# Kernel optimization log

Hardware: AMD Instinct MI355X
Metric: run time of the kernel (lower is better)

The kernel has to match this reference:

```python
import jax, jax.numpy as jnp
import numpy as np

B, S, D = 4, 2048, 1024
H, A = 16, 64  # num_heads, attention_depth
LN_EPS = 1e-3  # keras LayerNormalization default epsilon


def setup_inputs() -> dict:
    key = jax.random.key(0)
    ks = jax.random.split(key, 12)
    s_in = 1.0 / np.sqrt(D)
    return {
        "query_inputs": jax.random.normal(ks[0], (B, S, D), jnp.float32),
        "key_value_inputs": jax.random.normal(ks[1], (B, S, D), jnp.float32),
        "Wq": jax.random.normal(ks[2], (H, D, A), jnp.float32) * s_in,
        "bq": jnp.zeros((H, A), jnp.float32),
        "Wk": jax.random.normal(ks[3], (H, D, A), jnp.float32) * s_in,
        "bk": jnp.zeros((H, A), jnp.float32),
        "Wo": jax.random.normal(ks[4], (H, D, D), jnp.float32) * s_in,
        "bo": jnp.zeros((H, D), jnp.float32),
        "gamma": jnp.ones((D,), jnp.float32),
        "beta": jnp.zeros((D,), jnp.float32),
    }


def reference(query_inputs, key_value_inputs, Wq, bq, Wk, bk, Wo, bo, gamma, beta):
    sqrt_depth = jnp.sqrt(jnp.asarray(A, jnp.float32))
    # per-head Q/K projections, batched over heads: [B,H,S,A]
    q = (jnp.einsum("bsd,hda->bhsa", query_inputs, Wq) + bq[None, :, None, :]) / sqrt_depth
    k = jnp.einsum("btd,hda->bhta", key_value_inputs, Wk) + bk[None, :, None, :]
    # keras Attention: scores = q @ k^T (q already pre-scaled), causal mask
    scores = jnp.einsum("bhsa,bhta->bhst", q, k)
    causal = jnp.tril(jnp.ones((S, S), bool))
    scores = jnp.where(causal[None, None], scores, jnp.finfo(scores.dtype).min)
    weights = jax.nn.softmax(scores, axis=-1)
    # values are the raw key_value_inputs (model_dims channels)
    attn = jnp.einsum("bhst,btd->bhsd", weights, key_value_inputs)
    # per-head output dense with relu, then sum over heads (tf.add_n)
    head_out = jax.nn.relu(jnp.einsum("bhsd,hde->bhse", attn, Wo) + bo[None, :, None, :])
    attn_sum = head_out.sum(axis=1)  # [B,S,D]
    # dropout is identity in inference mode (training=False)
    x = query_inputs + attn_sum
    mean = x.mean(axis=-1, keepdims=True)
    var = x.var(axis=-1, keepdims=True)
    return gamma * (x - mean) * jax.lax.rsqrt(var + LN_EPS) + beta
```

## Files before the change

kernel.cpp:

```cpp
#include <hip/hip_runtime.h>
#include <stdint.h>

#define B_ 4
#define S_ 2048
#define D_ 1024
#define H_ 16
#define A_ 64
#define LN_EPS 1e-3f
#define L2E 1.4426950408889634f

typedef __bf16 bf16x8 __attribute__((ext_vector_type(8)));
typedef __bf16 bf16x4 __attribute__((ext_vector_type(4)));
typedef float f32x4 __attribute__((ext_vector_type(4)));

__device__ __forceinline__ f32x4 mfma16(bf16x8 a, bf16x8 b, f32x4 c) {
    return __builtin_amdgcn_mfma_f32_16x16x32_bf16(a, b, c, 0, 0, 0);
}
__device__ __forceinline__ void glds16(const void* g, void* l) {
    __builtin_amdgcn_global_load_lds(
        (const __attribute__((address_space(1))) void*)g,
        (__attribute__((address_space(3))) void*)l, 16, 0, 0);
}

#define SWZ(slot, r) ((slot) ^ (((r) & 1) << 2) ^ (((r) >> 1) & 3))
__device__ __forceinline__ void stage_half(const __bf16* __restrict__ src, size_t ld,
                                           __bf16* lhalf, int w, int lane) {
    #pragma unroll
    for (int i = 0; i < 2; ++i) {
        int ch = w * 2 + i;
        int r = ch * 8 + (lane >> 3);
        int sl = SWZ(lane & 7, r);
        glds16(src + (size_t)r * ld + sl * 8, lhalf + ch * 512);
    }
}
__device__ __forceinline__ bf16x8 fragS(const __bf16* h, int r, int ks, int fg) {
    return *(const bf16x8*)(h + r * 64 + SWZ(ks * 4 + fg, r) * 8);
}

__device__ __forceinline__ void glds_tile128(const __bf16* __restrict__ src, size_t ld,
                                             __bf16* lds, int w, int lane) {
    int r = lane >> 2;
    int c = (lane & 3) * 8;
    #pragma unroll
    for (int i = 0; i < 2; ++i) {
        int r0 = (w + i * 4) * 16;
        glds16(src + (size_t)(r0 + r) * ld + c, lds + r0 * 32);
    }
}
template <int NI, int NJ>
__device__ __forceinline__ void mfma_tileL(const __bf16* As, const __bf16* Bs,
                                           int wm, int wn, int fr, int fg,
                                           f32x4 (&acc)[NI][NJ]) {
    bf16x8 af[NI], bv[NJ];
    #pragma unroll
    for (int i = 0; i < NI; ++i)
        af[i] = *(const bf16x8*)(As + (wm + i * 16 + fr) * 32 + fg * 8);
    #pragma unroll
    for (int j = 0; j < NJ; ++j)
        bv[j] = *(const bf16x8*)(Bs + (wn + j * 16 + fr) * 32 + fg * 8);
    #pragma unroll
    for (int i = 0; i < NI; ++i)
        #pragma unroll
        for (int j = 0; j < NJ; ++j)
            acc[i][j] = mfma16(af[i], bv[j], acc[i][j]);
}

__global__ void k_tr_cvt(const float* __restrict__ in, __bf16* __restrict__ out,
                         int R, int C) {
    __shared__ float tile[32][33];
    size_t gbase = (size_t)blockIdx.z * R * C;
    int r0 = blockIdx.y * 32, c0 = blockIdx.x * 32;
    #pragma unroll
    for (int i = threadIdx.y; i < 32; i += 8)
        tile[i][threadIdx.x] = in[gbase + (size_t)(r0 + i) * C + c0 + threadIdx.x];
    __syncthreads();
    #pragma unroll
    for (int i = threadIdx.y; i < 32; i += 8)
        out[gbase + (size_t)(c0 + i) * R + r0 + threadIdx.x] = (__bf16)tile[threadIdx.x][i];
}
__global__ void k_tr_cvt2(const float* __restrict__ in0, const float* __restrict__ in1,
                          __bf16* __restrict__ out0, __bf16* __restrict__ out1,
                          int R, int C) {
    __shared__ float tile[32][33];
    int z = blockIdx.z;
    const float* in = (z < H_) ? in0 : in1;
    __bf16* out = (z < H_) ? out0 : out1;
    size_t gbase = (size_t)(z & (H_ - 1)) * R * C;
    int r0 = blockIdx.y * 32, c0 = blockIdx.x * 32;
    #pragma unroll
    for (int i = threadIdx.y; i < 32; i += 8)
        tile[i][threadIdx.x] = in[gbase + (size_t)(r0 + i) * C + c0 + threadIdx.x];
    __syncthreads();
    #pragma unroll
    for (int i = threadIdx.y; i < 32; i += 8)
        out[gbase + (size_t)(c0 + i) * R + r0 + threadIdx.x] = (__bf16)tile[threadIdx.x][i];
}

__global__ void k_cvt2(const float* __restrict__ in0, const float* __restrict__ in1,
                       __bf16* __restrict__ out0, __bf16* __restrict__ out1, int n8) {
    int i = blockIdx.x * blockDim.x + threadIdx.x;
    if (i >= n8) return;
    const float* in = blockIdx.y ? in1 : in0;
    __bf16* out = blockIdx.y ? out1 : out0;
    const float4* p = (const float4*)(in + (size_t)i * 8);
    float4 f0 = p[0], f1 = p[1];
    __bf16 v[8] = {(__bf16)f0.x, (__bf16)f0.y, (__bf16)f0.z, (__bf16)f0.w,
                   (__bf16)f1.x, (__bf16)f1.y, (__bf16)f1.z, (__bf16)f1.w};
    *(uint4*)(out + (size_t)i * 8) = *(const uint4*)v;
}

__global__ __launch_bounds__(256) void k_proj(
    const __bf16* __restrict__ qb, const __bf16* __restrict__ kvb,
    const __bf16* __restrict__ wqt, const __bf16* __restrict__ wkt,
    const float* __restrict__ bq, const float* __restrict__ bk,
    __bf16* __restrict__ qp, __bf16* __restrict__ kp) {
    __shared__ __bf16 As[2][128 * 32];
    __shared__ __bf16 Bs[2][128 * 32];
    int which = blockIdx.z;
    const __bf16* Ab = which ? kvb : qb;
    const __bf16* Bt = which ? wkt : wqt;
    const float* bias = which ? bk : bq;
    float scale = which ? 1.0f : 0.125f;
    __bf16* outp = which ? kp : qp;
    int m0 = blockIdx.y * 128, n0 = blockIdx.x * 128;
    int t = threadIdx.x, lane = t & 63, w = t >> 6;
    int wm = (w >> 1) * 64, wn = (w & 1) * 64;
    int fr = lane & 15, fg = lane >> 4;
    const __bf16* Abase = Ab + (size_t)m0 * D_;
    const __bf16* Bbase = Bt + (size_t)n0 * D_;
    f32x4 acc[4][4] = {};
    glds_tile128(Abase, D_, As[0], w, lane);
    glds_tile128(Bbase, D_, Bs[0], w, lane);
    __syncthreads();
    int cur = 0;
    const int nt = D_ / 32;
    for (int tt = 0; tt < nt; ++tt) {
        if (tt + 1 < nt) {
            glds_tile128(Abase + (tt + 1) * 32, D_, As[cur ^ 1], w, lane);
            glds_tile128(Bbase + (tt + 1) * 32, D_, Bs[cur ^ 1], w, lane);
        }
        mfma_tileL<4, 4>(As[cur], Bs[cur], wm, wn, fr, fg, acc);
        __syncthreads();
        cur ^= 1;
    }
    #pragma unroll
    for (int j = 0; j < 4; ++j) {
        int n = n0 + wn + j * 16 + fr;
        float bv = bias[n];
        #pragma unroll
        for (int i = 0; i < 4; ++i)
            #pragma unroll
            for (int jj = 0; jj < 4; ++jj) {
                int m = m0 + wm + i * 16 + fg * 4 + jj;
                outp[(size_t)m * (H_ * A_) + n] = (__bf16)((acc[i][j][jj] + bv) * scale);
            }
    }
}

__global__ __launch_bounds__(512) void k_fattn(
    const __bf16* __restrict__ qpb, const __bf16* __restrict__ kpb,
    const __bf16* __restrict__ kvtb, __bf16* __restrict__ att, int hb0) {
    __shared__ __bf16 Ks[2][64 * 64];
    __shared__ __bf16 Vs[2][2][128 * 64];
    __shared__ __bf16 Ps[128 * 64];
    __shared__ float lpar[128][2];
    int hl = blockIdx.z;
    int h = hb0 + hl;
    int yp = blockIdx.y;
    int n0 = blockIdx.x * 256;
    int t = threadIdx.x, lane = t & 63, w = t >> 6;
    int fr = lane & 15, fg = lane >> 4;
    int wr = w >> 2, wc = w & 3;
    int sr = w >> 1, sc = w & 1;
    const __bf16* Vb = kvtb + (size_t)n0 * S_;
    __bf16* ob = att + (size_t)hl * S_ * D_;

    #pragma unroll 1
    for (int seg = 0; seg < 2; ++seg) {
        int mt = seg ? (15 - yp) : yp;
        int m0 = mt * 128;
        int NT = (mt + 1) * 2;
        stage_half(qpb + (size_t)m0 * (H_ * A_) + h * A_, H_ * A_, Ps, w, lane);
        {
            int r = w * 8 + (lane >> 3);
            glds16(kpb + (size_t)r * (H_ * A_) + h * A_ + SWZ(lane & 7, r) * 8,
                   &Ks[0][w * 512]);
        }
        asm volatile("s_waitcnt vmcnt(0)" ::: "memory");
        __builtin_amdgcn_s_barrier();
        bf16x8 qf[2][2];
        #pragma unroll
        for (int mi = 0; mi < 2; ++mi)
            #pragma unroll
            for (int ks = 0; ks < 2; ++ks)
                qf[mi][ks] = fragS(Ps, sr * 32 + mi * 16 + fr, ks, fg);
        asm volatile("s_waitcnt lgkmcnt(0)" ::: "memory");
        stage_half(Vb, S_, &Vs[0][0][0], w, lane);
        stage_half(Vb + (size_t)128 * S_, S_, &Vs[0][1][0], w, lane);
        __builtin_amdgcn_s_barrier();
        __builtin_amdgcn_sched_barrier(0);
        f32x4 acc[4][4] = {};
        float lsum[2][4] = {};
        int cur = 0;
        for (int tt = 0; tt < NT; ++tt) {
            bool pre = (tt + 1 < NT);
            if (pre) {
                int r = w * 8 + (lane >> 3);
                glds16(kpb + (size_t)((tt + 1) * 64 + r) * (H_ * A_) + h * A_ +
                           SWZ(lane & 7, r) * 8,
                       &Ks[cur ^ 1][w * 512]);
                stage_half(Vb + (tt + 1) * 64, S_, &Vs[cur ^ 1][0][0], w, lane);
                stage_half(Vb + (size_t)128 * S_ + (tt + 1) * 64, S_,
                           &Vs[cur ^ 1][1][0], w, lane);
                asm volatile("s_waitcnt vmcnt(5)" ::: "memory");
            } else {
                asm volatile("s_waitcnt vmcnt(0)" ::: "memory");
            }
            __builtin_amdgcn_s_barrier();
            __builtin_amdgcn_sched_barrier(0);
            f32x4 sac[2][2] = {};
            __builtin_amdgcn_s_setprio(1);
            #pragma unroll
            for (int ks = 0; ks < 2; ++ks)
                #pragma unroll
                for (int nj = 0; nj < 2; ++nj) {
                    bf16x8 kf = fragS(&Ks[cur][0], sc * 32 + nj * 16 + fr, ks, fg);
                    #pragma unroll
                    for (int mi = 0; mi < 2; ++mi)
                        sac[mi][nj] = mfma16(qf[mi][ks], kf, sac[mi][nj]);
                }
            __builtin_amdgcn_s_setprio(0);
            bool dg = (tt >= 2 * mt);
            #pragma unroll
            for (int mi = 0; mi < 2; ++mi)
                #pragma unroll
                for (int nj = 0; nj < 2; ++nj)
                    #pragma unroll
                    for (int jj = 0; jj < 4; ++jj) {
                        int srow = sr * 32 + mi * 16 + fg * 4 + jj;
                        int col = sc * 32 + nj * 16 + fr;
                        float p = exp2f(sac[mi][nj][jj] * L2E);
                        if (dg && (tt * 64 + col > m0 + srow)) p = 0.f;
                        lsum[mi][jj] += p;
                        Ps[srow * 64 + (col ^ (fg << 4))] = (__bf16)p;
                    }
            asm volatile("s_waitcnt lgkmcnt(0)" ::: "memory");
            __builtin_amdgcn_s_barrier();
            __builtin_amdgcn_sched_barrier(0);
            __builtin_amdgcn_s_setprio(1);
            const __bf16* Vh = &Vs[cur][wc >> 1][0];
            #pragma unroll
            for (int ks = 0; ks < 2; ++ks) {
                bf16x8 pa[4], vf[4];
                #pragma unroll
                for (int mi = 0; mi < 4; ++mi) {
                    int r = wr * 64 + mi * 16 + fr;
                    int g = (ks * 4 + fg) ^ (((fr >> 2) & 3) << 1);
                    pa[mi] = *(const bf16x8*)(Ps + r * 64 + g * 8);
                }
                #pragma unroll
                for (int nj = 0; nj < 4; ++nj)
                    vf[nj] = fragS(Vh, (wc & 1) * 64 + nj * 16 + fr, ks, fg);
                #pragma unroll
                for (int mi = 0; mi < 4; ++mi)
                    #pragma unroll
                    for (int nj = 0; nj < 4; ++nj)
                        acc[mi][nj] = mfma16(pa[mi], vf[nj], acc[mi][nj]);
            }
            __builtin_amdgcn_s_setprio(0);
            __builtin_amdgcn_sched_barrier(0);
            cur ^= 1;
        }
        #pragma unroll
        for (int mi = 0; mi < 2; ++mi)
            #pragma unroll
            for (int jj = 0; jj < 4; ++jj) {
                float v = lsum[mi][jj];
                v += __shfl_xor(v, 1);
                v += __shfl_xor(v, 2);
                v += __shfl_xor(v, 4);
                v += __shfl_xor(v, 8);
                if (fr == 0) lpar[sr * 32 + mi * 16 + fg * 4 + jj][sc] = v;
            }
        asm volatile("s_waitcnt lgkmcnt(0)" ::: "memory");
        __builtin_amdgcn_s_barrier();
        #pragma unroll
        for (int mi = 0; mi < 4; ++mi)
            #pragma unroll
            for (int jj = 0; jj < 4; ++jj) {
                int row = wr * 64 + mi * 16 + fg * 4 + jj;
                float il = 1.f / (lpar[row][0] + lpar[row][1]);
                int m = m0 + row;
                #pragma unroll
                for (int nj = 0; nj < 4; ++nj) {
                    int n = n0 + wc * 64 + nj * 16 + fr;
                    ob[(size_t)m * D_ + n] = (__bf16)(acc[mi][nj][jj] * il);
                }
            }
        __builtin_amdgcn_s_barrier();
    }
}

__global__ __launch_bounds__(512) void k_headsum(
    const __bf16* __restrict__ att, const __bf16* __restrict__ Wot,
    const float* __restrict__ bo, __bf16* __restrict__ asum) {
    __shared__ __bf16 L[2][4][8192];
    int p = blockIdx.z;
    int mt = blockIdx.y, n0 = blockIdx.x * 256;
    int m0 = mt * 256;
    int t = threadIdx.x, lane = t & 63, w = t >> 6;
    int wr = w >> 2, wc = w & 3;
    int fr = lane & 15, fg = lane >> 4;
    const __bf16* Ab = att + ((size_t)p * S_ + m0) * D_;
    const __bf16* Bb = Wot + ((size_t)p * D_ + n0) * D_;
    float bv4[4];
    #pragma unroll
    for (int j = 0; j < 4; ++j)
        bv4[j] = bo[(size_t)p * D_ + n0 + wc * 64 + j * 16 + fr];
    f32x4 acc[8][4] = {};
    auto stg = [&](int tt, int h, int buf) {
        const __bf16* s = (h < 2) ? (Ab + (size_t)(h * 128) * D_ + tt * 64)
                                  : (Bb + (size_t)((h - 2) * 128) * D_ + tt * 64);
        stage_half(s, D_, &L[buf][h][0], w, lane);
    };
    auto loads = [&](const __bf16* Ah, const __bf16* Bh, int rb0, int mh, int nh,
                     bf16x8 (&af)[4][2], bf16x8 (&bv)[2][2]) {
        #pragma unroll
        for (int i = 0; i < 4; ++i)
            #pragma unroll
            for (int ks = 0; ks < 2; ++ks)
                af[i][ks] = fragS(Ah, mh * 64 + i * 16 + fr, ks, fg);
        #pragma unroll
        for (int j = 0; j < 2; ++j)
            #pragma unroll
            for (int ks = 0; ks < 2; ++ks)
                bv[j][ks] = fragS(Bh, rb0 + nh * 32 + j * 16 + fr, ks, fg);
    };
    stg(0, 0, 0); stg(0, 1, 0); stg(0, 2, 0); stg(0, 3, 0);
    int cur = 0;
    const int nt = D_ / 64;
    for (int tt = 0; tt < nt; ++tt) {
        bool pre = (tt + 1 < nt);
        const __bf16* Ah = &L[cur][wr][0];
        const __bf16* Bh = &L[cur][2 + (wc >> 1)][0];
        int rb0 = (wc & 1) * 64;
        #pragma unroll
        for (int ph = 0; ph < 4; ++ph) {
            const int mh = ph >> 1, nh = ph & 1;
            bf16x8 af[4][2], bv[2][2];
            if (ph == 0) {
                if (pre) {
                    stg(tt + 1, 0, cur ^ 1);
                    stg(tt + 1, 1, cur ^ 1);
                    stg(tt + 1, 2, cur ^ 1);
                    stg(tt + 1, 3, cur ^ 1);
                    asm volatile("s_waitcnt vmcnt(8)" ::: "memory");
                } else {
                    asm volatile("s_waitcnt vmcnt(0)" ::: "memory");
                }
                __builtin_amdgcn_s_barrier();
                __builtin_amdgcn_sched_barrier(0);
                loads(Ah, Bh, rb0, mh, nh, af, bv);
            } else {
                loads(Ah, Bh, rb0, mh, nh, af, bv);
                __builtin_amdgcn_s_barrier();
                __builtin_amdgcn_sched_barrier(0);
            }
            __builtin_amdgcn_s_setprio(1);
            #pragma unroll
            for (int i = 0; i < 4; ++i)
                #pragma unroll
                for (int j = 0; j < 2; ++j) {
                    acc[mh * 4 + i][nh * 2 + j] =
                        mfma16(af[i][0], bv[j][0], acc[mh * 4 + i][nh * 2 + j]);
                    acc[mh * 4 + i][nh * 2 + j] =
                        mfma16(af[i][1], bv[j][1], acc[mh * 4 + i][nh * 2 + j]);
                }
            __builtin_amdgcn_s_setprio(0);
            __builtin_amdgcn_sched_barrier(0);
            __builtin_amdgcn_s_barrier();
        }
        cur ^= 1;
    }
    __bf16* dst = asum + ((size_t)p * S_ + m0) * D_;
    #pragma unroll
    for (int mi = 0; mi < 8; ++mi)
        #pragma unroll
        for (int jj = 0; jj < 4; ++jj) {
            int mr = wr * 128 + mi * 16 + fg * 4 + jj;
            #pragma unroll
            for (int nj = 0; nj < 4; ++nj) {
                int nc = n0 + wc * 64 + nj * 16 + fr;
                dst[(size_t)mr * D_ + nc] = (__bf16)fmaxf(acc[mi][nj][jj] + bv4[nj], 0.f);
            }
        }
}

__global__ __launch_bounds__(256) void k_ln(
    const float* __restrict__ x1b, const __bf16* __restrict__ parts,
    const float* __restrict__ gamma, const float* __restrict__ beta,
    float* __restrict__ outb) {
    int row = blockIdx.x;
    size_t base = (size_t)row * D_;
    int c = threadIdx.x * 4;
    float4 a = *(const float4*)(x1b + base + c);
    float x[4] = {a.x, a.y, a.z, a.w};
    #pragma unroll
    for (int p = 0; p < H_; ++p) {
        bf16x4 v = *(const bf16x4*)(parts + ((size_t)p * S_ + row) * D_ + c);
        x[0] += (float)v[0]; x[1] += (float)v[1];
        x[2] += (float)v[2]; x[3] += (float)v[3];
    }
    float sm = x[0] + x[1] + x[2] + x[3];
    float s2 = x[0] * x[0] + x[1] * x[1] + x[2] * x[2] + x[3] * x[3];
    #pragma unroll
    for (int m = 32; m >= 1; m >>= 1) {
        sm += __shfl_xor(sm, m);
        s2 += __shfl_xor(s2, m);
    }
    __shared__ float r1[4], r2[4];
    int w = threadIdx.x >> 6;
    if ((threadIdx.x & 63) == 0) { r1[w] = sm; r2[w] = s2; }
    __syncthreads();
    sm = r1[0] + r1[1] + r1[2] + r1[3];
    s2 = r2[0] + r2[1] + r2[2] + r2[3];
    float mean = sm * (1.f / D_);
    float var = s2 * (1.f / D_) - mean * mean;
    float rstd = rsqrtf(var + LN_EPS);
    #pragma unroll
    for (int jj = 0; jj < 4; ++jj)
        outb[base + c + jj] = gamma[c + jj] * (x[jj] - mean) * rstd + beta[c + jj];
}

extern "C" void kernel_launch(void* const* d_in, const int* in_sizes, int n_in,
                              void* d_out, int out_size, void* d_ws, size_t ws_size,
                              hipStream_t stream) {
    (void)in_sizes; (void)n_in; (void)out_size; (void)ws_size;
    const float* qin   = (const float*)d_in[0];
    const float* kvin  = (const float*)d_in[1];
    const float* Wq    = (const float*)d_in[2];
    const float* bq    = (const float*)d_in[3];
    const float* Wk    = (const float*)d_in[4];
    const float* bk    = (const float*)d_in[5];
    const float* Wo    = (const float*)d_in[6];
    const float* bo    = (const float*)d_in[7];
    const float* gamma = (const float*)d_in[8];
    const float* beta  = (const float*)d_in[9];
    float* out = (float*)d_out;
    char* ws = (char*)d_ws;

    size_t off = 0;
    auto alloc = [&](size_t bytes) {
        size_t o = off;
        off += (bytes + 255) & ~(size_t)255;
        return o;
    };
    size_t o_wqt = alloc((size_t)H_ * A_ * D_ * 2);
    size_t o_wkt = alloc((size_t)H_ * A_ * D_ * 2);
    size_t o_wot = alloc((size_t)H_ * D_ * D_ * 2);
    size_t o_kvt = alloc((size_t)B_ * D_ * S_ * 2);
    size_t o_qp  = alloc((size_t)B_ * S_ * H_ * A_ * 2);
    size_t o_kp  = alloc((size_t)B_ * S_ * H_ * A_ * 2);
    size_t o_att = alloc((size_t)H_ * S_ * D_ * 2);
    size_t xbytes_qb = (size_t)B_ * S_ * D_ * 2 * 2;
    size_t xbytes_as = (size_t)H_ * S_ * D_ * 2;
    size_t o_x = alloc(xbytes_qb > xbytes_as ? xbytes_qb : xbytes_as);

    __bf16* wqt = (__bf16*)(ws + o_wqt);
    __bf16* wkt = (__bf16*)(ws + o_wkt);
    __bf16* wot = (__bf16*)(ws + o_wot);
    __bf16* kvt = (__bf16*)(ws + o_kvt);
    __bf16* qp  = (__bf16*)(ws + o_qp);
    __bf16* kp  = (__bf16*)(ws + o_kp);
    __bf16* att = (__bf16*)(ws + o_att);
    __bf16* qb  = (__bf16*)(ws + o_x);
    __bf16* kvb = qb + (size_t)B_ * S_ * D_;
    __bf16* asum = (__bf16*)(ws + o_x);

    k_tr_cvt2<<<dim3(A_ / 32, D_ / 32, 2 * H_), dim3(32, 8), 0, stream>>>(
        Wq, Wk, wqt, wkt, D_, A_);
    k_tr_cvt<<<dim3(D_ / 32, D_ / 32, H_), dim3(32, 8), 0, stream>>>(Wo, wot, D_, D_);
    k_tr_cvt<<<dim3(D_ / 32, S_ / 32, B_), dim3(32, 8), 0, stream>>>(kvin, kvt, S_, D_);
    int n8 = B_ * S_ * D_ / 8;
    k_cvt2<<<dim3((n8 + 255) / 256, 2), 256, 0, stream>>>(qin, kvin, qb, kvb, n8);
    k_proj<<<dim3(8, 64, 2), 256, 0, stream>>>(qb, kvb, wqt, wkt, bq, bk, qp, kp);

    for (int b = 0; b < B_; ++b) {
        const __bf16* qpb  = qp + (size_t)b * S_ * (H_ * A_);
        const __bf16* kpb  = kp + (size_t)b * S_ * (H_ * A_);
        const __bf16* kvtb = kvt + (size_t)b * D_ * S_;
        k_fattn<<<dim3(D_ / 256, 8, H_), 512, 0, stream>>>(qpb, kpb, kvtb, att, 0);
        k_headsum<<<dim3(D_ / 256, S_ / 256, H_), 512, 0, stream>>>(att, wot, bo, asum);
        k_ln<<<S_, 256, 0, stream>>>(qin + (size_t)b * S_ * D_, asum, gamma, beta,
                                     out + (size_t)b * S_ * D_);
    }
}
```

Baseline: 1.202 ms.

## Widen attention value tile to 512 columns and stage K through registers

The flash-attention kernel now covers 512 value columns per block instead of 256. This halves the number of blocks that recompute QK^T scores and softmax for the same head and row tile, and each wave accumulates a 4x8 grid of MFMA tiles. The next K tile is prefetched into a register and written into a single LDS buffer after the score phase, so K is no longer double-buffered in LDS. In exchange, register pressure rises (launch bounds of 512 threads with 1 block per CU) and the grid shrinks to half as many blocks, which could hurt occupancy and load balance.

```diff
diff --git a/kernel.cpp b/kernel.cpp
--- a/kernel.cpp
+++ b/kernel.cpp
@@ -157,23 +157,24 @@
     }
 }
 
-__global__ __launch_bounds__(512) void k_fattn(
+__global__ __launch_bounds__(512, 1) void k_fattn(
     const __bf16* __restrict__ qpb, const __bf16* __restrict__ kpb,
-    const __bf16* __restrict__ kvtb, __bf16* __restrict__ att, int hb0) {
-    __shared__ __bf16 Ks[2][64 * 64];
-    __shared__ __bf16 Vs[2][2][128 * 64];
+    const __bf16* __restrict__ kvtb, __bf16* __restrict__ att) {
+    __shared__ __bf16 Ks[64 * 64];
+    __shared__ __bf16 Vs[2][4][128 * 64];
     __shared__ __bf16 Ps[128 * 64];
     __shared__ float lpar[128][2];
-    int hl = blockIdx.z;
-    int h = hb0 + hl;
+    int h = blockIdx.z;
     int yp = blockIdx.y;
-    int n0 = blockIdx.x * 256;
+    int n0 = blockIdx.x * 512;
     int t = threadIdx.x, lane = t & 63, w = t >> 6;
     int fr = lane & 15, fg = lane >> 4;
     int wr = w >> 2, wc = w & 3;
     int sr = w >> 1, sc = w & 1;
     const __bf16* Vb = kvtb + (size_t)n0 * S_;
-    __bf16* ob = att + (size_t)hl * S_ * D_;
+    __bf16* ob = att + (size_t)h * S_ * D_;
+    int kr = w * 8 + (lane >> 3);
+    int ksl = SWZ(lane & 7, kr);
 
     #pragma unroll 1
     for (int seg = 0; seg < 2; ++seg) {
@@ -181,11 +182,7 @@
         int m0 = mt * 128;
         int NT = (mt + 1) * 2;
         stage_half(qpb + (size_t)m0 * (H_ * A_) + h * A_, H_ * A_, Ps, w, lane);
-        {
-            int r = w * 8 + (lane >> 3);
-            glds16(kpb + (size_t)r * (H_ * A_) + h * A_ + SWZ(lane & 7, r) * 8,
-                   &Ks[0][w * 512]);
-        }
+        glds16(kpb + (size_t)kr * (H_ * A_) + h * A_ + ksl * 8, Ks + w * 512);
         asm volatile("s_waitcnt vmcnt(0)" ::: "memory");
         __builtin_amdgcn_s_barrier();
         bf16x8 qf[2][2];
@@ -195,27 +192,25 @@
             for (int ks = 0; ks < 2; ++ks)
                 qf[mi][ks] = fragS(Ps, sr * 32 + mi * 16 + fr, ks, fg);
         asm volatile("s_waitcnt lgkmcnt(0)" ::: "memory");
-        stage_half(Vb, S_, &Vs[0][0][0], w, lane);
-        stage_half(Vb + (size_t)128 * S_, S_, &Vs[0][1][0], w, lane);
+        #pragma unroll
+        for (int q = 0; q < 4; ++q)
+            stage_half(Vb + (size_t)(q * 128) * S_, S_, &Vs[0][q][0], w, lane);
+        uint4 kreg = {0, 0, 0, 0};
+        if (NT > 1)
+            kreg = *(const uint4*)(kpb + (size_t)(64 + kr) * (H_ * A_) + h * A_ + ksl * 8);
         __builtin_amdgcn_s_barrier();
         __builtin_amdgcn_sched_barrier(0);
-        f32x4 acc[4][4] = {};
+        f32x4 acc[4][8] = {};
         float lsum[2][4] = {};
         int cur = 0;
         for (int tt = 0; tt < NT; ++tt) {
             bool pre = (tt + 1 < NT);
             if (pre) {
-                int r = w * 8 + (lane >> 3);
-                glds16(kpb + (size_t)((tt + 1) * 64 + r) * (H_ * A_) + h * A_ +
-                           SWZ(lane & 7, r) * 8,
-                       &Ks[cur ^ 1][w * 512]);
-                stage_half(Vb + (tt + 1) * 64, S_, &Vs[cur ^ 1][0][0], w, lane);
-                stage_half(Vb + (size_t)128 * S_ + (tt + 1) * 64, S_,
-                           &Vs[cur ^ 1][1][0], w, lane);
-                asm volatile("s_waitcnt vmcnt(5)" ::: "memory");
+                asm volatile("s_waitcnt vmcnt(1)" ::: "memory");
             } else {
                 asm volatile("s_waitcnt vmcnt(0)" ::: "memory");
             }
+            asm volatile("s_waitcnt lgkmcnt(0)" ::: "memory");
             __builtin_amdgcn_s_barrier();
             __builtin_amdgcn_sched_barrier(0);
             f32x4 sac[2][2] = {};
@@ -224,7 +219,7 @@
             for (int ks = 0; ks < 2; ++ks)
                 #pragma unroll
                 for (int nj = 0; nj < 2; ++nj) {
-                    bf16x8 kf = fragS(&Ks[cur][0], sc * 32 + nj * 16 + fr, ks, fg);
+                    bf16x8 kf = fragS(Ks, sc * 32 + nj * 16 + fr, ks, fg);
                     #pragma unroll
                     for (int mi = 0; mi < 2; ++mi)
                         sac[mi][nj] = mfma16(qf[mi][ks], kf, sac[mi][nj]);
@@ -247,11 +242,22 @@
             asm volatile("s_waitcnt lgkmcnt(0)" ::: "memory");
             __builtin_amdgcn_s_barrier();
             __builtin_amdgcn_sched_barrier(0);
+            if (pre) {
+                #pragma unroll
+                for (int q = 0; q < 4; ++q)
+                    stage_half(Vb + (size_t)(q * 128) * S_ + (tt + 1) * 64, S_,
+                               &Vs[cur ^ 1][q][0], w, lane);
+                asm volatile("s_waitcnt vmcnt(8)" ::: "memory");
+                *(uint4*)(Ks + w * 512 + lane * 8) = kreg;
+                if (tt + 2 < NT)
+                    kreg = *(const uint4*)(kpb + (size_t)((tt + 2) * 64 + kr) * (H_ * A_) +
+                                           h * A_ + ksl * 8);
+            }
             __builtin_amdgcn_s_setprio(1);
-            const __bf16* Vh = &Vs[cur][wc >> 1][0];
+            const __bf16* Vh = &Vs[cur][wc][0];
             #pragma unroll
             for (int ks = 0; ks < 2; ++ks) {
-                bf16x8 pa[4], vf[4];
+                bf16x8 pa[4], vf[8];
                 #pragma unroll
                 for (int mi = 0; mi < 4; ++mi) {
                     int r = wr * 64 + mi * 16 + fr;
@@ -259,12 +265,12 @@
                     pa[mi] = *(const bf16x8*)(Ps + r * 64 + g * 8);
                 }
                 #pragma unroll
-                for (int nj = 0; nj < 4; ++nj)
-                    vf[nj] = fragS(Vh, (wc & 1) * 64 + nj * 16 + fr, ks, fg);
+                for (int nj = 0; nj < 8; ++nj)
+                    vf[nj] = fragS(Vh, nj * 16 + fr, ks, fg);
                 #pragma unroll
                 for (int mi = 0; mi < 4; ++mi)
                     #pragma unroll
-                    for (int nj = 0; nj < 4; ++nj)
+                    for (int nj = 0; nj < 8; ++nj)
                         acc[mi][nj] = mfma16(pa[mi], vf[nj], acc[mi][nj]);
             }
             __builtin_amdgcn_s_setprio(0);
@@ -292,8 +298,8 @@
                 float il = 1.f / (lpar[row][0] + lpar[row][1]);
                 int m = m0 + row;
                 #pragma unroll
-                for (int nj = 0; nj < 4; ++nj) {
-                    int n = n0 + wc * 64 + nj * 16 + fr;
+                for (int nj = 0; nj < 8; ++nj) {
+                    int n = n0 + wc * 128 + nj * 16 + fr;
                     ob[(size_t)m * D_ + n] = (__bf16)(acc[mi][nj][jj] * il);
                 }
             }
@@ -489,7 +495,7 @@
         const __bf16* qpb  = qp + (size_t)b * S_ * (H_ * A_);
         const __bf16* kpb  = kp + (size_t)b * S_ * (H_ * A_);
         const __bf16* kvtb = kvt + (size_t)b * D_ * S_;
-        k_fattn<<<dim3(D_ / 256, 8, H_), 512, 0, stream>>>(qpb, kpb, kvtb, att, 0);
+        k_fattn<<<dim3(D_ / 512, 8, H_), 512, 0, stream>>>(qpb, kpb, kvtb, att);
         k_headsum<<<dim3(D_ / 256, S_ / 256, H_), 512, 0, stream>>>(att, wot, bo, asum);
         k_ln<<<S_, 256, 0, stream>>>(qin + (size_t)b * S_ * D_, asum, gamma, beta,
                                      out + (size_t)b * S_ * D_);
```

After: 1.143 ms. 4.9% less time.
